# Kernel tuning notes

Hardware: AMD Instinct MI355X
Metric: run time of the kernel (lower is better)

Reference implementation:

```python
import jax, jax.numpy as jnp
import numpy as np

B, N, DIM, HEADS = 8, 4096, 512, 8
BASE = 10000.0


def rope_cos_sin(n, dim, base=BASE):
    k_max = dim // 2
    theta = 1.0 / base ** (jnp.arange(k_max, dtype=jnp.float32) / k_max)
    angles = jnp.arange(n, dtype=jnp.float32)[:, None] * theta  # (n, k_max)
    return jnp.cos(angles), jnp.sin(angles)


def apply_rope(x, cos, sin):
    # x: (b, n, dim); complex pairs are interleaved (even=real, odd=imag)
    xr = x[..., 0::2]
    xi = x[..., 1::2]
    out_r = cos * xr - sin * xi
    out_i = sin * xr + cos * xi
    return jnp.stack([out_r, out_i], axis=-1).reshape(x.shape)


def setup_inputs() -> dict:
    key = jax.random.key(0)
    ks = jax.random.split(key, 8)
    s = 0.02
    return {
        'x': jax.random.normal(ks[0], (B, N, DIM), jnp.float32),
        'y': jax.random.normal(ks[1], (B, N, DIM), jnp.float32),
        'Wq': jax.random.normal(ks[2], (DIM, DIM), jnp.float32) * s,
        'bq': jax.random.normal(ks[3], (DIM,), jnp.float32) * s,
        'Wk': jax.random.normal(ks[4], (DIM, DIM), jnp.float32) * s,
        'bk': jax.random.normal(ks[5], (DIM,), jnp.float32) * s,
        'lepe_w': jax.random.normal(ks[6], (DIM, 1, 3), jnp.float32) * s,
        'lepe_b': jax.random.normal(ks[7], (DIM,), jnp.float32) * s,
    }


def reference(x, y, Wq, bq, Wk, bk, lepe_w, lepe_b):
    b, n, c = x.shape
    h = HEADS
    d = c // h
    q = jax.nn.elu(x @ Wq.T + bq) + 1.0
    k = jax.nn.elu(y @ Wk.T + bk) + 1.0
    cos, sin = rope_cos_sin(n, c)
    q_rope = apply_rope(q, cos, sin).reshape(b, n, h, d).transpose(0, 2, 1, 3)
    k_rope = apply_rope(k, cos, sin).reshape(b, n, h, d).transpose(0, 2, 1, 3)
    qh = q.reshape(b, n, h, d).transpose(0, 2, 1, 3)
    kh = k.reshape(b, n, h, d).transpose(0, 2, 1, 3)
    v = y.reshape(b, n, h, d).transpose(0, 2, 1, 3)
    kmean = kh.mean(axis=2, keepdims=True)  # (b,h,1,d)
    z = 1.0 / (jnp.einsum('bhnd,bhmd->bhnm', qh, kmean) + 1e-6)  # (b,h,n,1)
    scale = n ** (-0.5)
    kv = jnp.einsum('bhnd,bhne->bhde', k_rope * scale, v * scale)  # (b,h,d,d)
    out = jnp.einsum('bhnd,bhde->bhne', q_rope, kv) * z  # (b,h,n,d)
    out = out.transpose(0, 2, 1, 3).reshape(b, n, c)
    # LePE: depthwise conv1d over value stream
    vc = v.transpose(0, 2, 1, 3).reshape(b, n, c).transpose(0, 2, 1)  # (b,c,n)
    lepe = jax.lax.conv_general_dilated(
        vc, lepe_w, window_strides=(1,), padding=[(1, 1)],
        dimension_numbers=('NCH', 'OIH', 'NCH'), feature_group_count=c)
    lepe = lepe + lepe_b[None, :, None]
    return out + lepe.transpose(0, 2, 1)
```

## Files before the change

kernel.cpp:

```cpp
#include <hip/hip_runtime.h>

#define B_ 8
#define N_ 4096
#define C_ 512
#define H_ 8

typedef _Float16 h8  __attribute__((ext_vector_type(8)));
typedef _Float16 h4v __attribute__((ext_vector_type(4)));
typedef float    f4  __attribute__((ext_vector_type(4)));

static const size_t OFF_COS  = 0;
static const size_t OFF_SIN  = (size_t)4*1024*1024;
static const size_t OFF_KRH  = (size_t)8*1024*1024;
static const size_t OFF_WQH  = (size_t)40*1024*1024;
static const size_t OFF_WKH  = (size_t)40*1024*1024 + 512*1024;
static const size_t OFF_KSUM = (size_t)41*1024*1024;
static const size_t OFF_KVG  = (size_t)41*1024*1024 + 64*1024;
static const size_t OFF_KVT  = (size_t)42*1024*1024 + 64*1024;

__device__ __forceinline__ unsigned int pack2h(float a, float b){
    union { _Float16 h[2]; unsigned int u; } x;
    x.h[0] = (_Float16)a; x.h[1] = (_Float16)b; return x.u;
}

__global__ void k_tables(float* __restrict__ cosT, float* __restrict__ sinT){
    int n = blockIdx.x, j = threadIdx.x;
    double th = exp((double)j * -0.035977892078031970);
    float ang = (float)n * (float)th;
    float s, c; sincosf(ang, &s, &c);
    cosT[n*256 + j] = c; sinT[n*256 + j] = s;
}

__global__ __launch_bounds__(256) void k_prepw(const float* __restrict__ Wq, const float* __restrict__ Wk,
                                               _Float16* __restrict__ Wqh, _Float16* __restrict__ Wkh){
    int u = blockIdx.x*256 + threadIdx.x;
    {
        float4 a = *(const float4*)&Wq[(size_t)u*8];
        float4 b = *(const float4*)&Wq[(size_t)u*8 + 4];
        uint4 o; o.x = pack2h(a.x,a.y); o.y = pack2h(a.z,a.w); o.z = pack2h(b.x,b.y); o.w = pack2h(b.z,b.w);
        *(uint4*)&Wqh[(size_t)u*8] = o;
    }
    {
        float4 a = *(const float4*)&Wk[(size_t)u*8];
        float4 b = *(const float4*)&Wk[(size_t)u*8 + 4];
        uint4 o; o.x = pack2h(a.x,a.y); o.y = pack2h(a.z,a.w); o.z = pack2h(b.x,b.y); o.w = pack2h(b.z,b.w);
        *(uint4*)&Wkh[(size_t)u*8] = o;
    }
}

__device__ __forceinline__ void stage_b(const _Float16* __restrict__ g, _Float16* lds, int t){
#pragma unroll
    for (int i=0;i<2;++i){
        int u = i*256 + t;
        int r = u >> 2;
        int c8 = (u & 3) ^ ((r ^ (r >> 2)) & 3);
        __builtin_amdgcn_global_load_lds(
            (const __attribute__((address_space(1))) void*)(g + (size_t)r*C_ + c8*8),
            (__attribute__((address_space(3))) void*)(lds + (size_t)(i*256 + (t & 192))*8),
            16, 0, 0);
    }
}

template<int IS_Q>
__global__ __launch_bounds__(256, IS_Q ? 3 : 4) void k_gemm(
    const float* __restrict__ X, const _Float16* __restrict__ Wh, const float* __restrict__ bias,
    const float* __restrict__ cosT, const float* __restrict__ sinT,
    _Float16* __restrict__ krh, float* __restrict__ ksum,
    const float* __restrict__ ksumIn, const _Float16* __restrict__ kvTg,
    const float* __restrict__ y, const float* __restrict__ lw, const float* __restrict__ lb,
    float* __restrict__ outp)
{
    __shared__ __align__(16) char smem[IS_Q ? 53248 : 36864];
    _Float16* qrs = (_Float16*)smem;
    _Float16* kvs = (_Float16*)(smem + 36864);

    const int t = threadIdx.x;
    const int lane = t & 63;
    const int w = t >> 6;
    const int wm = w >> 1, wn = w & 1;
    const int col0 = blockIdx.x * 128;
    const int row0 = blockIdx.y * 128;
    const int lrow = lane & 15, lg = lane >> 4;
    const int srow = t >> 3;
    const int sc4 = (t & 7) * 4;
    const int b = row0 >> 12;

    f4 acc[4][4] = {};
    const float* Xp = X + (size_t)(row0 + srow)*C_ + sc4;
    float4 ra[4];
#pragma unroll
    for (int it=0; it<4; ++it) ra[it] = *(const float4*)(Xp + (size_t)it*32*C_);
    stage_b(Wh + (size_t)col0*C_, (_Float16*)(smem + 20480), t);

    const int sw = (lrow ^ (lrow >> 2)) & 3;
    const int cB = (lg ^ sw) * 8;
    int cur = 0;

    for (int kk=0; kk<16; ++kk){
        _Float16* As = (_Float16*)(smem + cur*10240);
#pragma unroll
        for (int it=0; it<4; ++it){
            int r = srow + it*32;
            h4v a; a[0]=(_Float16)ra[it].x; a[1]=(_Float16)ra[it].y; a[2]=(_Float16)ra[it].z; a[3]=(_Float16)ra[it].w;
            *(h4v*)&As[r*40 + sc4] = a;
        }
        __syncthreads();
        if (kk < 15){
#pragma unroll
            for (int it=0; it<4; ++it)
                ra[it] = *(const float4*)(Xp + (size_t)it*32*C_ + (kk+1)*32);
            stage_b(Wh + (size_t)col0*C_ + (kk+1)*32, (_Float16*)(smem + 20480 + (cur^1)*8192), t);
        }
        _Float16* Bs = (_Float16*)(smem + 20480 + cur*8192);
        h8 af[4], bf[4];
#pragma unroll
        for (int mi=0; mi<4; ++mi) af[mi] = *(const h8*)&As[(wm*64 + mi*16 + lrow)*40 + lg*8];
#pragma unroll
        for (int ni=0; ni<4; ++ni) bf[ni] = *(const h8*)&Bs[(wn*64 + ni*16 + lrow)*32 + cB];
#pragma unroll
        for (int mi=0; mi<4; ++mi)
#pragma unroll
            for (int ni=0; ni<4; ++ni)
                acc[mi][ni] = __builtin_amdgcn_mfma_f32_16x16x32_f16(af[mi], bf[ni], acc[mi][ni], 0,0,0);
        cur ^= 1;
    }
    __syncthreads();

    const int hcol0 = col0 + wn*64;
    if constexpr (IS_Q){
#pragma unroll
        for (int i=0;i<4;++i){
            int idx = i*256 + t;
            int hl = idx >> 9, e = (idx >> 3) & 63, u = idx & 7;
            int du = u ^ (e & 7);
            int bhh = b*H_ + (col0 >> 6) + hl;
            *(uint4*)&kvs[hl*4096 + e*64 + u*8] =
                *(const uint4*)&kvTg[(size_t)bhh*4096 + e*64 + du*8];
        }
    }
    float bcol[4], km[4];
#pragma unroll
    for (int ni=0; ni<4; ++ni){
        int c = hcol0 + ni*16 + lrow;
        bcol[ni] = bias[c];
        km[ni] = IS_Q ? ksumIn[b*C_ + c] * (1.0f/4096.0f) : 0.0f;
    }
    float colsum[4] = {0.f,0.f,0.f,0.f};
    float zr[4][4];
    _Float16* qw = qrs + w*4608;

#pragma unroll
    for (int mi=0; mi<4; ++mi){
        float qv[4][4];
#pragma unroll
        for (int ni=0; ni<4; ++ni)
#pragma unroll
            for (int r=0; r<4; ++r){
                float v = acc[mi][ni][r] + bcol[ni];
                qv[ni][r] = v > 0.f ? v + 1.f : __expf(v);
            }
        if constexpr (IS_Q){
#pragma unroll
            for (int r=0; r<4; ++r){
                float p = qv[0][r]*km[0] + qv[1][r]*km[1] + qv[2][r]*km[2] + qv[3][r]*km[3];
                p += __shfl_xor(p, 1); p += __shfl_xor(p, 2);
                p += __shfl_xor(p, 4); p += __shfl_xor(p, 8);
                zr[mi][r] = 1.0f / (p + 1e-6f);
            }
        } else {
#pragma unroll
            for (int ni=0; ni<4; ++ni)
                colsum[ni] += qv[ni][0]+qv[ni][1]+qv[ni][2]+qv[ni][3];
        }
#pragma unroll
        for (int ni=0; ni<4; ++ni){
            int c = hcol0 + ni*16 + lrow;
            int jj = c >> 1;
#pragma unroll
            for (int r=0; r<4; ++r){
                int grow = row0 + wm*64 + mi*16 + lg*4 + r;
                int n = grow & (N_-1);
                float val = qv[ni][r];
                float par = __shfl_xor(val, 1);
                float cs = cosT[n*256 + jj], sn = sinT[n*256 + jj];
                float rv = (lane & 1) ? fmaf(sn, par, cs*val) : fmaf(cs, val, -sn*par);
                float prv = __shfl_xor(rv, 1);
                if constexpr (IS_Q){
                    if (!(lane & 1))
                        *(unsigned int*)&qw[(mi*16 + lg*4 + r)*72 + (ni*16 + lrow)] = pack2h(rv, prv);
                } else {
                    if (!(lane & 1))
                        *(unsigned int*)&krh[(size_t)grow*C_ + c] = pack2h(rv, prv);
                }
            }
        }
    }

    if constexpr (!IS_Q){
#pragma unroll
        for (int ni=0; ni<4; ++ni){
            float s = colsum[ni];
            s += __shfl_xor(s, 16); s += __shfl_xor(s, 32);
            if (lane < 16) atomicAdd(&ksum[b*C_ + hcol0 + ni*16 + lane], s);
        }
    } else {
        __syncthreads();
        f4 acc2[4][4] = {};
#pragma unroll
        for (int ks=0; ks<2; ++ks){
            h8 af2[4], bf2[4];
#pragma unroll
            for (int mi2=0; mi2<4; ++mi2) af2[mi2] = *(const h8*)&qw[(mi2*16 + lrow)*72 + ks*32 + lg*8];
#pragma unroll
            for (int ni2=0; ni2<4; ++ni2){
                int e = ni2*16 + lrow;
                int du = ((ks*4 + lg) ^ (e & 7)) * 8;
                bf2[ni2] = *(const h8*)&kvs[wn*4096 + e*64 + du];
            }
#pragma unroll
            for (int mi2=0; mi2<4; ++mi2)
#pragma unroll
                for (int ni2=0; ni2<4; ++ni2)
                    acc2[mi2][ni2] = __builtin_amdgcn_mfma_f32_16x16x32_f16(af2[mi2], bf2[ni2], acc2[mi2][ni2], 0,0,0);
        }
#pragma unroll
        for (int mi2=0; mi2<4; ++mi2){
#pragma unroll
            for (int r=0; r<4; ++r){
                float z = zr[mi2][r];
#pragma unroll
                for (int ni2=0; ni2<4; ++ni2){
                    float val = acc2[mi2][ni2][r] * z;
                    float pv = __shfl_xor(val, 1);
                    if (!(lane & 1))
                        *(unsigned int*)&qw[(mi2*16 + lg*4 + r)*72 + (ni2*16 + lrow)] = pack2h(val, pv);
                }
            }
        }
        __syncthreads();
        const int cg = t & 31;
        const int c4p = cg * 4;
        const int hl = c4p >> 6;
        const int e0 = c4p & 63;
        float w0[4], w1[4], w2[4], wb[4];
#pragma unroll
        for (int j=0;j<4;++j){
            int cc = col0 + c4p + j;
            w0[j]=lw[cc*3+0]; w1[j]=lw[cc*3+1]; w2[j]=lw[cc*3+2]; wb[j]=lb[cc];
        }
#pragma unroll
        for (int i=0;i<16;++i){
            int rl = (t >> 5) + i*8;
            int grow = row0 + rl;
            int nloc = grow & (N_-1);
            int wreg = (rl >> 6)*2 + hl;
            h4v a = *(const h4v*)&qrs[wreg*4608 + (rl & 63)*72 + e0];
            const float* yp = y + (size_t)grow*C_ + col0 + c4p;
            float4 y1 = *(const float4*)yp;
            float s0 = fmaf(y1.x, w1[0], wb[0]);
            float s1 = fmaf(y1.y, w1[1], wb[1]);
            float s2 = fmaf(y1.z, w1[2], wb[2]);
            float s3 = fmaf(y1.w, w1[3], wb[3]);
            if (nloc > 0){
                float4 y0 = *(const float4*)(yp - C_);
                s0 = fmaf(y0.x, w0[0], s0); s1 = fmaf(y0.y, w0[1], s1);
                s2 = fmaf(y0.z, w0[2], s2); s3 = fmaf(y0.w, w0[3], s3);
            }
            if (nloc < N_-1){
                float4 y2 = *(const float4*)(yp + C_);
                s0 = fmaf(y2.x, w2[0], s0); s1 = fmaf(y2.y, w2[1], s1);
                s2 = fmaf(y2.z, w2[2], s2); s3 = fmaf(y2.w, w2[3], s3);
            }
            float4 o;
            o.x = (float)a[0] + s0; o.y = (float)a[1] + s1;
            o.z = (float)a[2] + s2; o.w = (float)a[3] + s3;
            *(float4*)&outp[(size_t)grow*C_ + col0 + c4p] = o;
        }
    }
}

__global__ __launch_bounds__(256) void k_kv(const _Float16* __restrict__ krh, const float* __restrict__ y,
                                            float* __restrict__ kvg){
    __shared__ _Float16 krs[64*128];
    __shared__ _Float16 vs[64*128];
    const int split = blockIdx.x, bh = blockIdx.y;
    const int b = bh >> 3, h = bh & 7;
    const int t = threadIdx.x, lane = t & 63, w = t >> 6;
    const int lrow = lane & 15, lg = lane >> 4;
    f4 acc[4] = {};
    for (int sub=0; sub<4; ++sub){
        const int n0 = split*512 + sub*128;
#pragma unroll
        for (int i=0;i<8;++i){
            int q = i*256 + t;
            int d2 = q & 31, n2 = q >> 5;
            int n = n0 + 2*n2, c = h*64 + 2*d2;
            size_t g0 = (size_t)(b*N_ + n)*C_ + c;
            unsigned int u0 = *(const unsigned int*)&krh[g0];
            unsigned int u1 = *(const unsigned int*)&krh[g0 + C_];
            int chunk = n2 >> 2, j2 = (n2 & 3)*2;
            int pc0 = chunk ^ ((2*d2) & 15);
            int pc1 = pc0 ^ 1;
            *(unsigned int*)&krs[(2*d2)*128 + pc0*8 + j2]   = (u0 & 0xffffu) | (u1 << 16);
            *(unsigned int*)&krs[(2*d2+1)*128 + pc1*8 + j2] = (u0 >> 16) | (u1 & 0xffff0000u);
            float2 a0 = *(const float2*)&y[g0];
            float2 a1 = *(const float2*)&y[g0 + C_];
            *(unsigned int*)&vs[(2*d2)*128 + pc0*8 + j2]   = pack2h(a0.x, a1.x);
            *(unsigned int*)&vs[(2*d2+1)*128 + pc1*8 + j2] = pack2h(a0.y, a1.y);
        }
        __syncthreads();
#pragma unroll
        for (int ks=0; ks<4; ++ks){
            int cu = ((ks*4 + lg) ^ lrow)*8;
            h8 a = *(const h8*)&krs[(w*16 + lrow)*128 + cu];
#pragma unroll
            for (int ni=0; ni<4; ++ni){
                h8 bv = *(const h8*)&vs[(ni*16 + lrow)*128 + cu];
                acc[ni] = __builtin_amdgcn_mfma_f32_16x16x32_f16(a, bv, acc[ni], 0,0,0);
            }
        }
        __syncthreads();
    }
#pragma unroll
    for (int ni=0; ni<4; ++ni)
#pragma unroll
        for (int rr=0; rr<4; ++rr)
            atomicAdd(&kvg[(size_t)bh*4096 + (w*16 + lg*4 + rr)*64 + ni*16 + lrow],
                      acc[ni][rr] * (1.0f/4096.0f));
}

__global__ __launch_bounds__(256) void k_kvmerge(const float* __restrict__ kvg, _Float16* __restrict__ kvTg){
    int bh = blockIdx.x, t = threadIdx.x;
    const float* src = kvg + (size_t)bh*4096;
    _Float16* dst = kvTg + (size_t)bh*4096;
#pragma unroll
    for (int i=0;i<4;++i){
        int q = i*256 + t;
        int e2 = q & 31, d2 = q >> 5;
        float2 a0 = *(const float2*)&src[(2*d2)*64 + 2*e2];
        float2 a1 = *(const float2*)&src[(2*d2+1)*64 + 2*e2];
        *(unsigned int*)&dst[(2*e2)*64 + 2*d2]   = pack2h(a0.x, a1.x);
        *(unsigned int*)&dst[(2*e2+1)*64 + 2*d2] = pack2h(a0.y, a1.y);
    }
}

extern "C" void kernel_launch(void* const* d_in, const int* in_sizes, int n_in,
                              void* d_out, int out_size, void* d_ws, size_t ws_size,
                              hipStream_t stream)
{
    (void)in_sizes; (void)n_in; (void)out_size; (void)ws_size;
    const float* x  = (const float*)d_in[0];
    const float* y  = (const float*)d_in[1];
    const float* Wq = (const float*)d_in[2];
    const float* bq = (const float*)d_in[3];
    const float* Wk = (const float*)d_in[4];
    const float* bk = (const float*)d_in[5];
    const float* lw = (const float*)d_in[6];
    const float* lb = (const float*)d_in[7];

    char* ws = (char*)d_ws;
    float*    cosT = (float*)(ws + OFF_COS);
    float*    sinT = (float*)(ws + OFF_SIN);
    _Float16* krh  = (_Float16*)(ws + OFF_KRH);
    _Float16* Wqh  = (_Float16*)(ws + OFF_WQH);
    _Float16* Wkh  = (_Float16*)(ws + OFF_WKH);
    float*    ksum = (float*)(ws + OFF_KSUM);
    float*    kvg  = (float*)(ws + OFF_KVG);
    _Float16* kvTg = (_Float16*)(ws + OFF_KVT);
    float*    out  = (float*)d_out;

    hipMemsetAsync(ws + OFF_KSUM, 0, 64*1024 + 1024*1024, stream);
    k_tables<<<dim3(N_), dim3(256), 0, stream>>>(cosT, sinT);
    k_prepw<<<dim3(128), dim3(256), 0, stream>>>(Wq, Wk, Wqh, Wkh);
    k_gemm<0><<<dim3(4, 256), dim3(256), 0, stream>>>(y, Wkh, bk, cosT, sinT,
        krh, ksum, nullptr, nullptr, nullptr, nullptr, nullptr, nullptr);
    k_kv<<<dim3(8, 64), dim3(256), 0, stream>>>(krh, y, kvg);
    k_kvmerge<<<dim3(64), dim3(256), 0, stream>>>(kvg, kvTg);
    k_gemm<1><<<dim3(4, 256), dim3(256), 0, stream>>>(x, Wqh, bq, cosT, sinT,
        nullptr, nullptr, ksum, kvTg, y, lw, lb, out);
}
```

Before: 214.7 us.

## Pre-convert activations to fp16 and stage both GEMM operands via direct-to-LDS loads

Adds conversion kernels that turn y, x and the weights into fp16 buffers. x is written into the krh buffer once k_kv has finished with it. Both GEMM operands are then staged with global_load_lds double buffering instead of register loads and conversion in the main loop, and the kvT tile is prefetched asynchronously before the loop. k_kv and the LePE path now read the fp16 y, which halves their read traffic. The cost is extra full-tensor conversion passes over x and y. LePE also loses some precision from reading fp16 values.

```diff
diff --git a/kernel.cpp b/kernel.cpp
--- a/kernel.cpp
+++ b/kernel.cpp
@@ -12,11 +12,12 @@
 static const size_t OFF_COS  = 0;
 static const size_t OFF_SIN  = (size_t)4*1024*1024;
 static const size_t OFF_KRH  = (size_t)8*1024*1024;
-static const size_t OFF_WQH  = (size_t)40*1024*1024;
-static const size_t OFF_WKH  = (size_t)40*1024*1024 + 512*1024;
-static const size_t OFF_KSUM = (size_t)41*1024*1024;
-static const size_t OFF_KVG  = (size_t)41*1024*1024 + 64*1024;
-static const size_t OFF_KVT  = (size_t)42*1024*1024 + 64*1024;
+static const size_t OFF_YH   = (size_t)40*1024*1024;
+static const size_t OFF_WQH  = (size_t)72*1024*1024;
+static const size_t OFF_WKH  = (size_t)72*1024*1024 + 512*1024;
+static const size_t OFF_KSUM = (size_t)73*1024*1024;
+static const size_t OFF_KVG  = (size_t)73*1024*1024 + 64*1024;
+static const size_t OFF_KVT  = (size_t)74*1024*1024 + 64*1024;
 
 __device__ __forceinline__ unsigned int pack2h(float a, float b){
     union { _Float16 h[2]; unsigned int u; } x;
@@ -31,31 +32,38 @@
     cosT[n*256 + j] = c; sinT[n*256 + j] = s;
 }
 
-__global__ __launch_bounds__(256) void k_prepw(const float* __restrict__ Wq, const float* __restrict__ Wk,
-                                               _Float16* __restrict__ Wqh, _Float16* __restrict__ Wkh){
-    int u = blockIdx.x*256 + threadIdx.x;
-    {
-        float4 a = *(const float4*)&Wq[(size_t)u*8];
-        float4 b = *(const float4*)&Wq[(size_t)u*8 + 4];
-        uint4 o; o.x = pack2h(a.x,a.y); o.y = pack2h(a.z,a.w); o.z = pack2h(b.x,b.y); o.w = pack2h(b.z,b.w);
-        *(uint4*)&Wqh[(size_t)u*8] = o;
-    }
-    {
-        float4 a = *(const float4*)&Wk[(size_t)u*8];
-        float4 b = *(const float4*)&Wk[(size_t)u*8 + 4];
-        uint4 o; o.x = pack2h(a.x,a.y); o.y = pack2h(a.z,a.w); o.z = pack2h(b.x,b.y); o.w = pack2h(b.z,b.w);
-        *(uint4*)&Wkh[(size_t)u*8] = o;
-    }
-}
-
-__device__ __forceinline__ void stage_b(const _Float16* __restrict__ g, _Float16* lds, int t){
+__global__ __launch_bounds__(256) void k_prep_y(
+    const float* __restrict__ y, const float* __restrict__ Wq, const float* __restrict__ Wk,
+    _Float16* __restrict__ yh, _Float16* __restrict__ Wqh, _Float16* __restrict__ Wkh)
+{
+    int bid = blockIdx.x;
+    const float* src; _Float16* dst; size_t base;
+    if (bid < 8192)      { src = y;  dst = yh;  base = (size_t)bid*2048; }
+    else if (bid < 8320) { src = Wq; dst = Wqh; base = (size_t)(bid-8192)*2048; }
+    else                 { src = Wk; dst = Wkh; base = (size_t)(bid-8320)*2048; }
+    size_t o = base + (size_t)threadIdx.x*8;
+    float4 a = *(const float4*)&src[o];
+    float4 b = *(const float4*)&src[o+4];
+    uint4 r; r.x = pack2h(a.x,a.y); r.y = pack2h(a.z,a.w); r.z = pack2h(b.x,b.y); r.w = pack2h(b.z,b.w);
+    *(uint4*)&dst[o] = r;
+}
+
+__global__ __launch_bounds__(256) void k_prep_x(const float* __restrict__ x, _Float16* __restrict__ xh){
+    size_t o = (size_t)blockIdx.x*2048 + (size_t)threadIdx.x*8;
+    float4 a = *(const float4*)&x[o];
+    float4 b = *(const float4*)&x[o+4];
+    uint4 r; r.x = pack2h(a.x,a.y); r.y = pack2h(a.z,a.w); r.z = pack2h(b.x,b.y); r.w = pack2h(b.z,b.w);
+    *(uint4*)&xh[o] = r;
+}
+
+__device__ __forceinline__ void stage_tile(const _Float16* __restrict__ g, _Float16* lds, int t){
 #pragma unroll
     for (int i=0;i<2;++i){
         int u = i*256 + t;
         int r = u >> 2;
-        int c8 = (u & 3) ^ ((r ^ (r >> 2)) & 3);
+        int j = (u & 3) ^ ((r ^ (r >> 2)) & 3);
         __builtin_amdgcn_global_load_lds(
-            (const __attribute__((address_space(1))) void*)(g + (size_t)r*C_ + c8*8),
+            (const __attribute__((address_space(1))) void*)(g + (size_t)r*C_ + j*8),
             (__attribute__((address_space(3))) void*)(lds + (size_t)(i*256 + (t & 192))*8),
             16, 0, 0);
     }
@@ -63,14 +71,14 @@
 
 template<int IS_Q>
 __global__ __launch_bounds__(256, IS_Q ? 3 : 4) void k_gemm(
-    const float* __restrict__ X, const _Float16* __restrict__ Wh, const float* __restrict__ bias,
+    const _Float16* __restrict__ A, const _Float16* __restrict__ Wh, const float* __restrict__ bias,
     const float* __restrict__ cosT, const float* __restrict__ sinT,
     _Float16* __restrict__ krh, float* __restrict__ ksum,
     const float* __restrict__ ksumIn, const _Float16* __restrict__ kvTg,
-    const float* __restrict__ y, const float* __restrict__ lw, const float* __restrict__ lb,
+    const _Float16* __restrict__ yh, const float* __restrict__ lw, const float* __restrict__ lb,
     float* __restrict__ outp)
 {
-    __shared__ __align__(16) char smem[IS_Q ? 53248 : 36864];
+    __shared__ __align__(16) char smem[IS_Q ? 53248 : 32768];
     _Float16* qrs = (_Float16*)smem;
     _Float16* kvs = (_Float16*)(smem + 36864);
 
@@ -81,63 +89,53 @@
     const int col0 = blockIdx.x * 128;
     const int row0 = blockIdx.y * 128;
     const int lrow = lane & 15, lg = lane >> 4;
-    const int srow = t >> 3;
-    const int sc4 = (t & 7) * 4;
     const int b = row0 >> 12;
 
+    if constexpr (IS_Q){
+#pragma unroll
+        for (int i=0;i<4;++i){
+            int idx = i*256 + t;
+            int hl = idx >> 9, w9 = idx & 511, e = w9 >> 3, u8 = w9 & 7;
+            int j = u8 ^ (e & 7);
+            int bhh = b*H_ + (col0 >> 6) + hl;
+            __builtin_amdgcn_global_load_lds(
+                (const __attribute__((address_space(1))) void*)(kvTg + (size_t)bhh*4096 + e*64 + j*8),
+                (__attribute__((address_space(3))) void*)(kvs + (size_t)(i*256 + (t & 192))*8),
+                16, 0, 0);
+        }
+    }
+
     f4 acc[4][4] = {};
-    const float* Xp = X + (size_t)(row0 + srow)*C_ + sc4;
-    float4 ra[4];
-#pragma unroll
-    for (int it=0; it<4; ++it) ra[it] = *(const float4*)(Xp + (size_t)it*32*C_);
-    stage_b(Wh + (size_t)col0*C_, (_Float16*)(smem + 20480), t);
+    stage_tile(A  + (size_t)row0*C_, (_Float16*)(smem), t);
+    stage_tile(Wh + (size_t)col0*C_, (_Float16*)(smem + 16384), t);
 
     const int sw = (lrow ^ (lrow >> 2)) & 3;
-    const int cB = (lg ^ sw) * 8;
+    const int cK = (lg ^ sw) * 8;
     int cur = 0;
 
     for (int kk=0; kk<16; ++kk){
-        _Float16* As = (_Float16*)(smem + cur*10240);
-#pragma unroll
-        for (int it=0; it<4; ++it){
-            int r = srow + it*32;
-            h4v a; a[0]=(_Float16)ra[it].x; a[1]=(_Float16)ra[it].y; a[2]=(_Float16)ra[it].z; a[3]=(_Float16)ra[it].w;
-            *(h4v*)&As[r*40 + sc4] = a;
-        }
         __syncthreads();
         if (kk < 15){
-#pragma unroll
-            for (int it=0; it<4; ++it)
-                ra[it] = *(const float4*)(Xp + (size_t)it*32*C_ + (kk+1)*32);
-            stage_b(Wh + (size_t)col0*C_ + (kk+1)*32, (_Float16*)(smem + 20480 + (cur^1)*8192), t);
-        }
-        _Float16* Bs = (_Float16*)(smem + 20480 + cur*8192);
+            stage_tile(A  + (size_t)row0*C_ + (kk+1)*32, (_Float16*)(smem + (cur^1)*8192), t);
+            stage_tile(Wh + (size_t)col0*C_ + (kk+1)*32, (_Float16*)(smem + 16384 + (cur^1)*8192), t);
+        }
+        const _Float16* As = (const _Float16*)(smem + cur*8192);
+        const _Float16* Bs = (const _Float16*)(smem + 16384 + cur*8192);
         h8 af[4], bf[4];
 #pragma unroll
-        for (int mi=0; mi<4; ++mi) af[mi] = *(const h8*)&As[(wm*64 + mi*16 + lrow)*40 + lg*8];
-#pragma unroll
-        for (int ni=0; ni<4; ++ni) bf[ni] = *(const h8*)&Bs[(wn*64 + ni*16 + lrow)*32 + cB];
+        for (int mi=0; mi<4; ++mi) af[mi] = *(const h8*)&As[(wm*64 + mi*16 + lrow)*32 + cK];
+#pragma unroll
+        for (int ni=0; ni<4; ++ni) bf[ni] = *(const h8*)&Bs[(wn*64 + ni*16 + lrow)*32 + cK];
 #pragma unroll
         for (int mi=0; mi<4; ++mi)
 #pragma unroll
             for (int ni=0; ni<4; ++ni)
                 acc[mi][ni] = __builtin_amdgcn_mfma_f32_16x16x32_f16(af[mi], bf[ni], acc[mi][ni], 0,0,0);
+        __syncthreads();
         cur ^= 1;
     }
-    __syncthreads();
 
     const int hcol0 = col0 + wn*64;
-    if constexpr (IS_Q){
-#pragma unroll
-        for (int i=0;i<4;++i){
-            int idx = i*256 + t;
-            int hl = idx >> 9, e = (idx >> 3) & 63, u = idx & 7;
-            int du = u ^ (e & 7);
-            int bhh = b*H_ + (col0 >> 6) + hl;
-            *(uint4*)&kvs[hl*4096 + e*64 + u*8] =
-                *(const uint4*)&kvTg[(size_t)bhh*4096 + e*64 + du*8];
-        }
-    }
     float bcol[4], km[4];
 #pragma unroll
     for (int ni=0; ni<4; ++ni){
@@ -255,21 +253,21 @@
             int nloc = grow & (N_-1);
             int wreg = (rl >> 6)*2 + hl;
             h4v a = *(const h4v*)&qrs[wreg*4608 + (rl & 63)*72 + e0];
-            const float* yp = y + (size_t)grow*C_ + col0 + c4p;
-            float4 y1 = *(const float4*)yp;
-            float s0 = fmaf(y1.x, w1[0], wb[0]);
-            float s1 = fmaf(y1.y, w1[1], wb[1]);
-            float s2 = fmaf(y1.z, w1[2], wb[2]);
-            float s3 = fmaf(y1.w, w1[3], wb[3]);
+            const _Float16* yp = yh + (size_t)grow*C_ + col0 + c4p;
+            h4v y1 = *(const h4v*)yp;
+            float s0 = fmaf((float)y1[0], w1[0], wb[0]);
+            float s1 = fmaf((float)y1[1], w1[1], wb[1]);
+            float s2 = fmaf((float)y1[2], w1[2], wb[2]);
+            float s3 = fmaf((float)y1[3], w1[3], wb[3]);
             if (nloc > 0){
-                float4 y0 = *(const float4*)(yp - C_);
-                s0 = fmaf(y0.x, w0[0], s0); s1 = fmaf(y0.y, w0[1], s1);
-                s2 = fmaf(y0.z, w0[2], s2); s3 = fmaf(y0.w, w0[3], s3);
+                h4v y0 = *(const h4v*)(yp - C_);
+                s0 = fmaf((float)y0[0], w0[0], s0); s1 = fmaf((float)y0[1], w0[1], s1);
+                s2 = fmaf((float)y0[2], w0[2], s2); s3 = fmaf((float)y0[3], w0[3], s3);
             }
             if (nloc < N_-1){
-                float4 y2 = *(const float4*)(yp + C_);
-                s0 = fmaf(y2.x, w2[0], s0); s1 = fmaf(y2.y, w2[1], s1);
-                s2 = fmaf(y2.z, w2[2], s2); s3 = fmaf(y2.w, w2[3], s3);
+                h4v y2 = *(const h4v*)(yp + C_);
+                s0 = fmaf((float)y2[0], w2[0], s0); s1 = fmaf((float)y2[1], w2[1], s1);
+                s2 = fmaf((float)y2[2], w2[2], s2); s3 = fmaf((float)y2[3], w2[3], s3);
             }
             float4 o;
             o.x = (float)a[0] + s0; o.y = (float)a[1] + s1;
@@ -279,7 +277,7 @@
     }
 }
 
-__global__ __launch_bounds__(256) void k_kv(const _Float16* __restrict__ krh, const float* __restrict__ y,
+__global__ __launch_bounds__(256) void k_kv(const _Float16* __restrict__ krh, const _Float16* __restrict__ yh,
                                             float* __restrict__ kvg){
     __shared__ _Float16 krs[64*128];
     __shared__ _Float16 vs[64*128];
@@ -298,15 +296,15 @@
             size_t g0 = (size_t)(b*N_ + n)*C_ + c;
             unsigned int u0 = *(const unsigned int*)&krh[g0];
             unsigned int u1 = *(const unsigned int*)&krh[g0 + C_];
+            unsigned int v0 = *(const unsigned int*)&yh[g0];
+            unsigned int v1 = *(const unsigned int*)&yh[g0 + C_];
             int chunk = n2 >> 2, j2 = (n2 & 3)*2;
             int pc0 = chunk ^ ((2*d2) & 15);
             int pc1 = pc0 ^ 1;
             *(unsigned int*)&krs[(2*d2)*128 + pc0*8 + j2]   = (u0 & 0xffffu) | (u1 << 16);
             *(unsigned int*)&krs[(2*d2+1)*128 + pc1*8 + j2] = (u0 >> 16) | (u1 & 0xffff0000u);
-            float2 a0 = *(const float2*)&y[g0];
-            float2 a1 = *(const float2*)&y[g0 + C_];
-            *(unsigned int*)&vs[(2*d2)*128 + pc0*8 + j2]   = pack2h(a0.x, a1.x);
-            *(unsigned int*)&vs[(2*d2+1)*128 + pc1*8 + j2] = pack2h(a0.y, a1.y);
+            *(unsigned int*)&vs[(2*d2)*128 + pc0*8 + j2]    = (v0 & 0xffffu) | (v1 << 16);
+            *(unsigned int*)&vs[(2*d2+1)*128 + pc1*8 + j2]  = (v0 >> 16) | (v1 & 0xffff0000u);
         }
         __syncthreads();
 #pragma unroll
@@ -362,6 +360,7 @@
     float*    cosT = (float*)(ws + OFF_COS);
     float*    sinT = (float*)(ws + OFF_SIN);
     _Float16* krh  = (_Float16*)(ws + OFF_KRH);
+    _Float16* yh   = (_Float16*)(ws + OFF_YH);
     _Float16* Wqh  = (_Float16*)(ws + OFF_WQH);
     _Float16* Wkh  = (_Float16*)(ws + OFF_WKH);
     float*    ksum = (float*)(ws + OFF_KSUM);
@@ -371,11 +370,12 @@
 
     hipMemsetAsync(ws + OFF_KSUM, 0, 64*1024 + 1024*1024, stream);
     k_tables<<<dim3(N_), dim3(256), 0, stream>>>(cosT, sinT);
-    k_prepw<<<dim3(128), dim3(256), 0, stream>>>(Wq, Wk, Wqh, Wkh);
-    k_gemm<0><<<dim3(4, 256), dim3(256), 0, stream>>>(y, Wkh, bk, cosT, sinT,
+    k_prep_y<<<dim3(8448), dim3(256), 0, stream>>>(y, Wq, Wk, yh, Wqh, Wkh);
+    k_gemm<0><<<dim3(4, 256), dim3(256), 0, stream>>>(yh, Wkh, bk, cosT, sinT,
         krh, ksum, nullptr, nullptr, nullptr, nullptr, nullptr, nullptr);
-    k_kv<<<dim3(8, 64), dim3(256), 0, stream>>>(krh, y, kvg);
+    k_kv<<<dim3(8, 64), dim3(256), 0, stream>>>(krh, yh, kvg);
     k_kvmerge<<<dim3(64), dim3(256), 0, stream>>>(kvg, kvTg);
-    k_gemm<1><<<dim3(4, 256), dim3(256), 0, stream>>>(x, Wqh, bq, cosT, sinT,
-        nullptr, nullptr, ksum, kvTg, y, lw, lb, out);
-}
+    k_prep_x<<<dim3(8192), dim3(256), 0, stream>>>(x, krh);
+    k_gemm<1><<<dim3(4, 256), dim3(256), 0, stream>>>(krh, Wqh, bq, cosT, sinT,
+        nullptr, nullptr, ksum, kvTg, yh, lw, lb, out);
+}
```

New measurement: 210.7 us. About the same (-1.9%).
